# Kernel tuning notes

Hardware: AMD Instinct MI355X
Metric: run time of the kernel (lower is better)

Reference implementation:

```python
import jax, jax.numpy as jnp
import numpy as np

N = 100000      # nodes
E = 1600000     # edges
F_IN = 128
HID = 128
N_CLS = 40
KEEP = 0.5      # 1 - dropout p
NORM_BIAS = 0.0


def setup_inputs() -> dict:
    key = jax.random.key(0)
    ks = jax.random.split(key, 12)
    features = jax.random.normal(ks[0], (N, F_IN), jnp.float32)
    src = jax.random.randint(ks[1], (E,), 0, N, jnp.int32)
    dst = jax.random.randint(ks[2], (E,), 0, N, jnp.int32)
    mask1 = jax.random.randint(ks[3], (N, HID), 0, 2) == 1
    mask2 = jax.random.randint(ks[4], (N, HID), 0, 2) == 1
    # Glorot-ish weights, zero bias (as in DGL GraphConv defaults)
    w0 = jax.random.normal(ks[5], (F_IN, HID), jnp.float32) / np.sqrt(F_IN)
    b0 = jnp.zeros((HID,), jnp.float32)
    w1 = jax.random.normal(ks[6], (HID, HID), jnp.float32) / np.sqrt(HID)
    b1 = jnp.zeros((HID,), jnp.float32)
    w2 = jax.random.normal(ks[7], (HID, N_CLS), jnp.float32) / np.sqrt(HID)
    b2 = jnp.zeros((N_CLS,), jnp.float32)
    return {"features": features, "src": src, "dst": dst,
            "mask1": mask1, "mask2": mask2,
            "w0": w0, "b0": b0, "w1": w1, "b1": b1, "w2": w2, "b2": b2}


def _graph_conv(h, w, b, src, dst, norm, act):
    # GraphConv: linear -> SpMM (sum over in-edges) -> right norm -> bias -> act
    h = h @ w                                       # [N, d_out]
    agg = jax.ops.segment_sum(h[src], dst, num_segments=N)  # copy_u/sum SpMM
    h = agg * norm[:, None] + b
    return jax.nn.relu(h) if act else h


def reference(features, src, dst, mask1, mask2, w0, b0, w1, b1, w2, b2):
    # right normalization: 1 / (in_degree + norm_bias), degree clamped to >= 1
    deg = jax.ops.segment_sum(jnp.ones((E,), jnp.float32), dst, num_segments=N)
    norm = 1.0 / (jnp.maximum(deg, 1.0) + NORM_BIAS)

    h = _graph_conv(features, w0, b0, src, dst, norm, act=True)
    h = jnp.where(mask1, h / KEEP, 0.0)   # dropout (inverted, deterministic mask)
    h = _graph_conv(h, w1, b1, src, dst, norm, act=True)
    h = jnp.where(mask2, h / KEEP, 0.0)
    h = _graph_conv(h, w2, b2, src, dst, norm, act=False)
    return h
```

## Files before the change

### kernel.cpp

```cpp
#include <hip/hip_runtime.h>


#define PAD 64

__device__ __forceinline__ unsigned short f2bf(float f) {
    unsigned u = __float_as_uint(f);
    return (unsigned short)((u + 0x7fffu + ((u >> 16) & 1u)) >> 16);
}

__global__ __launch_bounds__(256) void k_init(int* __restrict__ cnt, int n,
                                              const unsigned* __restrict__ m,
                                              int* __restrict__ flag) {
    int base = blockIdx.x * 1024 + threadIdx.x * 4;
#pragma unroll
    for (int j = 0; j < 4; ++j) {
        int i = base + j;
        if (i < n) cnt[i] = 0;
    }
    if (blockIdx.x < 4) {
        unsigned v = m[blockIdx.x * 256 + threadIdx.x];
        if (v > 1u) atomicOr(flag, 1);
    }
}

__global__ __launch_bounds__(256) void k_g0scat(
        const float* __restrict__ X, const float* __restrict__ Wg,
        unsigned short* __restrict__ Y, int nrows, int gb,
        const int* __restrict__ src, const int* __restrict__ dst,
        int* __restrict__ cnt, int* __restrict__ slots, int E) {
    __shared__ float Xs[64][32];
    __shared__ float Ws[32][128];
    int bid = blockIdx.x;
    int t = threadIdx.x;

    bool isg = (bid < gb * 5) && ((bid % 5) == 4);
    if (!isg) {
        int sblk = (bid < gb * 5) ? (bid / 5) * 4 + (bid % 5)
                                  : gb * 4 + (bid - gb * 5);
        int e = sblk * 256 + t;
        if (e < E) {
            int d = dst[e];
            int p = atomicAdd(&cnt[d], 1);
            if (p < PAD) slots[(size_t)d * PAD + p] = src[e];
        }
        return;
    }

    int bm = (bid / 5) * 64;
    int tx = t & 15, ty = t >> 4;
    int sw = ((ty >> 1) & 3) << 2;
    float acc[4][8];
#pragma unroll
    for (int i = 0; i < 4; ++i)
#pragma unroll
        for (int j = 0; j < 8; ++j) acc[i][j] = 0.0f;

    for (int kc = 0; kc < 128; kc += 32) {
        for (int idx = t; idx < 64 * 8; idx += 256) {
            int row = idx >> 3, k4 = idx & 7;
            int grow = bm + row;
            if (grow >= nrows) grow = nrows - 1;
            float4 v = *(const float4*)(X + (size_t)grow * 128 + kc + k4 * 4);
            int kk2 = (k4 * 4) ^ (((row >> 3) & 3) << 2);
            *(float4*)&Xs[row][kk2] = v;
        }
        for (int idx = t; idx < 32 * 32; idx += 256) {
            int k = idx >> 5, c4 = idx & 31;
            *(float4*)&Ws[k][c4 * 4] =
                *(const float4*)(Wg + (size_t)(kc + k) * 128 + c4 * 4);
        }
        __syncthreads();

        for (int k = 0; k < 32; k += 4) {
            float4 a4[4];
#pragma unroll
            for (int i = 0; i < 4; ++i)
                a4[i] = *(const float4*)&Xs[ty * 4 + i][k ^ sw];
#pragma unroll
            for (int kk = 0; kk < 4; ++kk) {
                float b[8];
                *(float4*)&b[0] = *(const float4*)&Ws[k + kk][tx * 4];
                *(float4*)&b[4] = *(const float4*)&Ws[k + kk][64 + tx * 4];
#pragma unroll
                for (int i = 0; i < 4; ++i) {
                    float a = ((const float*)&a4[i])[kk];
#pragma unroll
                    for (int j = 0; j < 8; ++j) acc[i][j] += a * b[j];
                }
            }
        }
        __syncthreads();
    }

#pragma unroll
    for (int i = 0; i < 4; ++i) {
        int r = bm + ty * 4 + i;
        if (r < nrows) {
            ushort4 u0, u1;
            u0.x = f2bf(acc[i][0]); u0.y = f2bf(acc[i][1]);
            u0.z = f2bf(acc[i][2]); u0.w = f2bf(acc[i][3]);
            u1.x = f2bf(acc[i][4]); u1.y = f2bf(acc[i][5]);
            u1.z = f2bf(acc[i][6]); u1.w = f2bf(acc[i][7]);
            *(ushort4*)(Y + (size_t)r * 128 + tx * 4) = u0;
            *(ushort4*)(Y + (size_t)r * 128 + 64 + tx * 4) = u1;
        }
    }
}

template<int BN, bool PACK>
__global__ __launch_bounds__(256, 3) void k_gemm(const float* __restrict__ X,
                                                 const float* __restrict__ Wg,
                                                 unsigned short* __restrict__ Y,
                                                 int nrows, int wcols) {
    constexpr int TN = BN / 16;
    __shared__ float Xs[128][32];
    __shared__ float Ws[32][BN];
    int t = threadIdx.x;
    int bm = blockIdx.x * 128;
    int tx = t & 15, ty = t >> 4;
    int sw = (ty & 3) << 2;

    float acc[8][TN];
#pragma unroll
    for (int i = 0; i < 8; ++i)
#pragma unroll
        for (int j = 0; j < TN; ++j) acc[i][j] = 0.0f;

    for (int kc = 0; kc < 128; kc += 32) {
        for (int idx = t; idx < 128 * 8; idx += 256) {
            int row = idx >> 3, k4 = idx & 7;
            int grow = bm + row;
            if (grow >= nrows) grow = nrows - 1;
            float4 v = *(const float4*)(X + (size_t)grow * 128 + kc + k4 * 4);
            int kk2 = (k4 * 4) ^ (((row >> 3) & 3) << 2);
            *(float4*)&Xs[row][kk2] = v;
        }
        if (BN == 128) {
            for (int idx = t; idx < 32 * 32; idx += 256) {
                int k = idx >> 5, c4 = idx & 31;
                *(float4*)&Ws[k][c4 * 4] =
                    *(const float4*)(Wg + (size_t)(kc + k) * 128 + c4 * 4);
            }
        } else {
            for (int idx = t; idx < 32 * BN; idx += 256) {
                int k = idx / BN, c = idx % BN;
                Ws[k][c] = (c < wcols) ? Wg[(size_t)(kc + k) * wcols + c] : 0.0f;
            }
        }
        __syncthreads();

        for (int k = 0; k < 32; k += 4) {
            float4 a4[8];
#pragma unroll
            for (int i = 0; i < 8; ++i)
                a4[i] = *(const float4*)&Xs[ty * 8 + i][k ^ sw];
#pragma unroll
            for (int kk = 0; kk < 4; ++kk) {
                float b[TN];
                *(float4*)&b[0] = *(const float4*)&Ws[k + kk][tx * 4];
                if (BN == 128)
                    *(float4*)&b[4] = *(const float4*)&Ws[k + kk][64 + tx * 4];
#pragma unroll
                for (int i = 0; i < 8; ++i) {
                    float a = ((const float*)&a4[i])[kk];
#pragma unroll
                    for (int j = 0; j < TN; ++j) acc[i][j] += a * b[j];
                }
            }
        }
        __syncthreads();
    }

    int ld = PACK ? wcols : BN;
#pragma unroll
    for (int i = 0; i < 8; ++i) {
        int r = bm + ty * 8 + i;
        if (r < nrows) {
            if (!PACK || tx * 4 < 40) {
                ushort4 u;
                u.x = f2bf(acc[i][0]); u.y = f2bf(acc[i][1]);
                u.z = f2bf(acc[i][2]); u.w = f2bf(acc[i][3]);
                *(ushort4*)(Y + (size_t)r * ld + tx * 4) = u;
            }
            if (BN == 128) {
                ushort4 u;
                u.x = f2bf(acc[i][4]); u.y = f2bf(acc[i][5]);
                u.z = f2bf(acc[i][6]); u.w = f2bf(acc[i][7]);
                *(ushort4*)(Y + (size_t)r * ld + 64 + tx * 4) = u;
            }
        }
    }
}

template<bool ACT>
__global__ __launch_bounds__(256) void k_spmmw(const unsigned* __restrict__ Y,
                       const int* __restrict__ cnt, const int* __restrict__ slots,
                       const float* __restrict__ bias,
                       const void* __restrict__ mask, const int* __restrict__ mflag,
                       float* __restrict__ H, int N) {
    int wid = threadIdx.x >> 6;
    int lane = threadIdx.x & 63;
    int i = blockIdx.x * 4 + wid;
    if (i >= N) return;
    int c = lane * 2;
    int d0 = cnt[i];
    int d = d0 > PAD ? PAD : d0;
    const int* row = slots + (size_t)i * PAD;
    float2 acc = {0.0f, 0.0f};
    int e = 0;
    for (; e + 3 < d; e += 4) {
        unsigned u0 = Y[(size_t)row[e] * 64 + lane];
        unsigned u1 = Y[(size_t)row[e + 1] * 64 + lane];
        unsigned u2 = Y[(size_t)row[e + 2] * 64 + lane];
        unsigned u3 = Y[(size_t)row[e + 3] * 64 + lane];
        acc.x += __uint_as_float(u0 << 16) + __uint_as_float(u1 << 16)
               + __uint_as_float(u2 << 16) + __uint_as_float(u3 << 16);
        acc.y += __uint_as_float(u0 & 0xffff0000u) + __uint_as_float(u1 & 0xffff0000u)
               + __uint_as_float(u2 & 0xffff0000u) + __uint_as_float(u3 & 0xffff0000u);
    }
    for (; e < d; ++e) {
        unsigned u = Y[(size_t)row[e] * 64 + lane];
        acc.x += __uint_as_float(u << 16);
        acc.y += __uint_as_float(u & 0xffff0000u);
    }
    float nrm = 1.0f / fmaxf((float)d0, 1.0f);
    float2 b = *(const float2*)&bias[c];
    float vx = acc.x * nrm + b.x;
    float vy = acc.y * nrm + b.y;
    if (ACT) {
        vx = fmaxf(vx, 0.0f);
        vy = fmaxf(vy, 0.0f);
        size_t j = (size_t)i * 128 + c;
        bool k0, k1;
        if (*mflag != 0) {
            const unsigned char* m = (const unsigned char*)mask;
            k0 = m[j] != 0; k1 = m[j + 1] != 0;
        } else {
            const int* m = (const int*)mask;
            k0 = m[j] != 0; k1 = m[j + 1] != 0;
        }
        vx = k0 ? vx * 2.0f : 0.0f;
        vy = k1 ? vy * 2.0f : 0.0f;
    }
    *(float2*)(H + (size_t)i * 128 + c) = make_float2(vx, vy);
}

__global__ __launch_bounds__(256) void k_spmm40w(const unsigned* __restrict__ Y,
                        const int* __restrict__ cnt, const int* __restrict__ slots,
                        const float* __restrict__ bias,
                        float* __restrict__ H, int N, int width) {
    int wid = threadIdx.x >> 6;
    int lane = threadIdx.x & 63;
    int i = blockIdx.x * 4 + wid;
    if (i >= N) return;
    int c = lane * 2;
    if (c >= width) return;
    int d0 = cnt[i];
    int d = d0 > PAD ? PAD : d0;
    const int* row = slots + (size_t)i * PAD;
    float2 acc = {0.0f, 0.0f};
    int e = 0;
    for (; e + 3 < d; e += 4) {
        unsigned u0 = Y[(size_t)row[e] * 20 + lane];
        unsigned u1 = Y[(size_t)row[e + 1] * 20 + lane];
        unsigned u2 = Y[(size_t)row[e + 2] * 20 + lane];
        unsigned u3 = Y[(size_t)row[e + 3] * 20 + lane];
        acc.x += __uint_as_float(u0 << 16) + __uint_as_float(u1 << 16)
               + __uint_as_float(u2 << 16) + __uint_as_float(u3 << 16);
        acc.y += __uint_as_float(u0 & 0xffff0000u) + __uint_as_float(u1 & 0xffff0000u)
               + __uint_as_float(u2 & 0xffff0000u) + __uint_as_float(u3 & 0xffff0000u);
    }
    for (; e < d; ++e) {
        unsigned u = Y[(size_t)row[e] * 20 + lane];
        acc.x += __uint_as_float(u << 16);
        acc.y += __uint_as_float(u & 0xffff0000u);
    }
    float nrm = 1.0f / fmaxf((float)d0, 1.0f);
    float vx = acc.x * nrm + bias[c];
    float vy = acc.y * nrm + bias[c + 1];
    *(float2*)(H + (size_t)i * width + c) = make_float2(vx, vy);
}

extern "C" void kernel_launch(void* const* d_in, const int* in_sizes, int n_in,
                              void* d_out, int out_size, void* d_ws, size_t ws_size,
                              hipStream_t stream) {
    const float* feat = (const float*)d_in[0];
    const int* src = (const int*)d_in[1];
    const int* dst = (const int*)d_in[2];
    const void* mask1 = d_in[3];
    const void* mask2 = d_in[4];
    const float* w0 = (const float*)d_in[5];
    const float* b0 = (const float*)d_in[6];
    const float* w1 = (const float*)d_in[7];
    const float* b1 = (const float*)d_in[8];
    const float* w2 = (const float*)d_in[9];
    const float* b2 = (const float*)d_in[10];
    int N = in_sizes[0] / 128;
    int E = in_sizes[1];
    int ncls = in_sizes[10];

    float* out = (float*)d_out;
    unsigned short* Y = (unsigned short*)d_ws;
    float* H = (float*)(Y + (size_t)N * 128);
    int* slots = (int*)(H + (size_t)N * 128);
    int* cnt = slots + (size_t)N * PAD;
    int* mflag = cnt + N;

    int nb = (N + 1023) / 1024;

    hipMemsetAsync(mflag, 0, 4, stream);
    k_init<<<nb, 256, 0, stream>>>(cnt, N, (const unsigned*)mask1, mflag);

    int eb = (E + 255) / 256;
    int gb64 = (N + 63) / 64;
    int scap = gb64 * 4;
    int extra = (eb > scap) ? (eb - scap) : 0;
    k_g0scat<<<gb64 * 5 + extra, 256, 0, stream>>>(feat, w0, Y, N, gb64,
                                                   src, dst, cnt, slots, E);

    int gb = (N + 127) / 128;
    int sb = (N + 3) / 4;
    k_spmmw<true><<<sb, 256, 0, stream>>>((const unsigned*)Y, cnt, slots, b0, mask1, mflag, H, N);
    k_gemm<128, false><<<gb, 256, 0, stream>>>(H, w1, Y, N, 128);
    k_spmmw<true><<<sb, 256, 0, stream>>>((const unsigned*)Y, cnt, slots, b1, mask2, mflag, H, N);
    k_gemm<64, true><<<gb, 256, 0, stream>>>(H, w2, Y, N, ncls);
    k_spmm40w<<<sb, 256, 0, stream>>>((const unsigned*)Y, cnt, slots, b2, out, N, ncls);
}
```

Measured before the change: 440.3 us.

## Shard edge scatter by destination range aligned to XCDs for L2 locality

Edge bucketing is restructured so each scatter block handles a 2048-edge window but only inserts edges whose destination lies in one of 8 node shards. The shard is picked as bid%8, which appears to line up with round-robin block placement across the 8 XCDs, so each XCD's atomics and slot writes stay within its own L2 slice. The cost is that every edge's dst is read 8 times, once per shard, and the block-to-window mapping becomes more complex. The hardcoded shard size of 12500 ties correctness to N=100000; for any larger N, nodes beyond the last shard would never be inserted.

```diff
diff --git a/kernel.cpp b/kernel.cpp
--- a/kernel.cpp
+++ b/kernel.cpp
@@ -2,6 +2,9 @@
 
 
 #define PAD 64
+#define NSHARD 8
+#define SHARD_DIV 12500
+#define WIN 2048
 
 __device__ __forceinline__ unsigned short f2bf(float f) {
     unsigned u = __float_as_uint(f);
@@ -25,7 +28,7 @@
 
 __global__ __launch_bounds__(256) void k_g0scat(
         const float* __restrict__ X, const float* __restrict__ Wg,
-        unsigned short* __restrict__ Y, int nrows, int gb,
+        unsigned short* __restrict__ Y, int nrows, int nwin,
         const int* __restrict__ src, const int* __restrict__ dst,
         int* __restrict__ cnt, int* __restrict__ slots, int E) {
     __shared__ float Xs[64][32];
@@ -33,20 +36,32 @@
     int bid = blockIdx.x;
     int t = threadIdx.x;
 
-    bool isg = (bid < gb * 5) && ((bid % 5) == 4);
-    if (!isg) {
-        int sblk = (bid < gb * 5) ? (bid / 5) * 4 + (bid % 5)
-                                  : gb * 4 + (bid - gb * 5);
-        int e = sblk * 256 + t;
-        if (e < E) {
-            int d = dst[e];
-            int p = atomicAdd(&cnt[d], 1);
-            if (p < PAD) slots[(size_t)d * PAD + p] = src[e];
+    if ((bid % 5) != 4) {
+        int q = bid % 40;
+        int rank = 0;
+        for (int j = bid % 8; j < q; j += 8)
+            if ((j % 5) != 4) ++rank;
+        int w = (bid / 40) * 4 + rank;
+        if (w >= nwin) return;
+        int shard = bid % 8;
+        int lo = shard * SHARD_DIV, hi = lo + SHARD_DIV;
+        int base = w * WIN + t;
+#pragma unroll
+        for (int k = 0; k < 8; ++k) {
+            int e = base + k * 256;
+            if (e < E) {
+                int d = dst[e];
+                if (d >= lo && d < hi) {
+                    int p = atomicAdd(&cnt[d], 1);
+                    if (p < PAD) slots[(size_t)d * PAD + p] = src[e];
+                }
+            }
         }
         return;
     }
 
     int bm = (bid / 5) * 64;
+    if (bm >= nrows) return;
     int tx = t & 15, ty = t >> 4;
     int sw = ((ty >> 1) & 3) << 2;
     float acc[4][8];
@@ -311,12 +326,13 @@
     hipMemsetAsync(mflag, 0, 4, stream);
     k_init<<<nb, 256, 0, stream>>>(cnt, N, (const unsigned*)mask1, mflag);
 
-    int eb = (E + 255) / 256;
+    int nwin = (E + WIN - 1) / WIN;
     int gb64 = (N + 63) / 64;
-    int scap = gb64 * 4;
-    int extra = (eb > scap) ? (eb - scap) : 0;
-    k_g0scat<<<gb64 * 5 + extra, 256, 0, stream>>>(feat, w0, Y, N, gb64,
-                                                   src, dst, cnt, slots, E);
+    int sp1 = (nwin * 8 + 31) / 32;
+    int sp2 = (gb64 + 7) / 8;
+    int sp = sp1 > sp2 ? sp1 : sp2;
+    k_g0scat<<<sp * 40, 256, 0, stream>>>(feat, w0, Y, N, nwin,
+                                          src, dst, cnt, slots, E);
 
     int gb = (N + 127) / 128;
     int sb = (N + 3) / 4;
```

Measured after the change: 436.1 us. About the same (-1.0%).

## Fuse SpMM aggregation with following dense GEMM via shared-memory tile

Applied to the files above, without the earlier changes.

Replaces the separate SpMM kernel (which wrote an fp32 H matrix) and the following GEMM kernel with a single kernel. Each block aggregates 64 destination rows, applies norm, bias, ReLU and the dropout mask, and stores the result in a swizzled 64x128 shared tile. It then multiplies that tile by the weight matrix and writes bf16 output. This removes the global write and re-read of the N x 128 fp32 intermediate and two launches. The cost is larger shared memory per block (32KB+), which lowers occupancy for the latency-bound gather phase, and smaller GEMM tiles.

```diff
diff --git a/kernel.cpp b/kernel.cpp
--- a/kernel.cpp
+++ b/kernel.cpp
@@ -107,34 +107,76 @@
     }
 }
 
-template<int BN, bool PACK>
-__global__ __launch_bounds__(256, 3) void k_gemm(const float* __restrict__ X,
-                                                 const float* __restrict__ Wg,
-                                                 unsigned short* __restrict__ Y,
-                                                 int nrows, int wcols) {
+template<int BN>
+__global__ __launch_bounds__(256) void k_spgemm(
+        const unsigned* __restrict__ Yin,
+        const int* __restrict__ cnt, const int* __restrict__ slots,
+        const float* __restrict__ bias,
+        const void* __restrict__ mask, const int* __restrict__ mflag,
+        const float* __restrict__ Wg,
+        unsigned short* __restrict__ Yout, int N, int wcols) {
     constexpr int TN = BN / 16;
-    __shared__ float Xs[128][32];
+    __shared__ float Xs[64][128];
     __shared__ float Ws[32][BN];
     int t = threadIdx.x;
-    int bm = blockIdx.x * 128;
+    int bm = blockIdx.x * 64;
+    int wid = t >> 6, lane = t & 63;
+    int c = lane * 2;
+    bool bytemask = (*mflag != 0);
+
+    for (int n = 0; n < 16; ++n) {
+        int row = wid * 16 + n;
+        int i = bm + row;
+        if (i >= N) break;
+        int d0 = cnt[i];
+        int d = d0 > PAD ? PAD : d0;
+        const int* rw = slots + (size_t)i * PAD;
+        float2 acc = {0.0f, 0.0f};
+        int e = 0;
+        for (; e + 3 < d; e += 4) {
+            unsigned u0 = Yin[(size_t)rw[e] * 64 + lane];
+            unsigned u1 = Yin[(size_t)rw[e + 1] * 64 + lane];
+            unsigned u2 = Yin[(size_t)rw[e + 2] * 64 + lane];
+            unsigned u3 = Yin[(size_t)rw[e + 3] * 64 + lane];
+            acc.x += __uint_as_float(u0 << 16) + __uint_as_float(u1 << 16)
+                   + __uint_as_float(u2 << 16) + __uint_as_float(u3 << 16);
+            acc.y += __uint_as_float(u0 & 0xffff0000u) + __uint_as_float(u1 & 0xffff0000u)
+                   + __uint_as_float(u2 & 0xffff0000u) + __uint_as_float(u3 & 0xffff0000u);
+        }
+        for (; e < d; ++e) {
+            unsigned u = Yin[(size_t)rw[e] * 64 + lane];
+            acc.x += __uint_as_float(u << 16);
+            acc.y += __uint_as_float(u & 0xffff0000u);
+        }
+        float nrm = 1.0f / fmaxf((float)d0, 1.0f);
+        float2 b = *(const float2*)&bias[c];
+        float vx = fmaxf(acc.x * nrm + b.x, 0.0f);
+        float vy = fmaxf(acc.y * nrm + b.y, 0.0f);
+        size_t j = (size_t)i * 128 + c;
+        bool k0, k1;
+        if (bytemask) {
+            const unsigned char* m = (const unsigned char*)mask;
+            k0 = m[j] != 0; k1 = m[j + 1] != 0;
+        } else {
+            const int* m = (const int*)mask;
+            k0 = m[j] != 0; k1 = m[j + 1] != 0;
+        }
+        vx = k0 ? vx * 2.0f : 0.0f;
+        vy = k1 ? vy * 2.0f : 0.0f;
+        int swr = ((row >> 2) & 3) << 2;
+        *(float2*)&Xs[row][c ^ swr] = make_float2(vx, vy);
+    }
+    __syncthreads();
+
     int tx = t & 15, ty = t >> 4;
     int sw = (ty & 3) << 2;
-
-    float acc[8][TN];
-#pragma unroll
-    for (int i = 0; i < 8; ++i)
+    float acc[4][TN];
+#pragma unroll
+    for (int i = 0; i < 4; ++i)
 #pragma unroll
         for (int j = 0; j < TN; ++j) acc[i][j] = 0.0f;
 
     for (int kc = 0; kc < 128; kc += 32) {
-        for (int idx = t; idx < 128 * 8; idx += 256) {
-            int row = idx >> 3, k4 = idx & 7;
-            int grow = bm + row;
-            if (grow >= nrows) grow = nrows - 1;
-            float4 v = *(const float4*)(X + (size_t)grow * 128 + kc + k4 * 4);
-            int kk2 = (k4 * 4) ^ (((row >> 3) & 3) << 2);
-            *(float4*)&Xs[row][kk2] = v;
-        }
         if (BN == 128) {
             for (int idx = t; idx < 32 * 32; idx += 256) {
                 int k = idx >> 5, c4 = idx & 31;
@@ -143,17 +185,17 @@
             }
         } else {
             for (int idx = t; idx < 32 * BN; idx += 256) {
-                int k = idx / BN, c = idx % BN;
-                Ws[k][c] = (c < wcols) ? Wg[(size_t)(kc + k) * wcols + c] : 0.0f;
+                int k = idx / BN, cc = idx % BN;
+                Ws[k][cc] = (cc < wcols) ? Wg[(size_t)(kc + k) * wcols + cc] : 0.0f;
             }
         }
         __syncthreads();
 
         for (int k = 0; k < 32; k += 4) {
-            float4 a4[8];
-#pragma unroll
-            for (int i = 0; i < 8; ++i)
-                a4[i] = *(const float4*)&Xs[ty * 8 + i][k ^ sw];
+            float4 a4[4];
+#pragma unroll
+            for (int i = 0; i < 4; ++i)
+                a4[i] = *(const float4*)&Xs[ty * 4 + i][(kc + k) ^ sw];
 #pragma unroll
             for (int kk = 0; kk < 4; ++kk) {
                 float b[TN];
@@ -161,7 +203,7 @@
                 if (BN == 128)
                     *(float4*)&b[4] = *(const float4*)&Ws[k + kk][64 + tx * 4];
 #pragma unroll
-                for (int i = 0; i < 8; ++i) {
+                for (int i = 0; i < 4; ++i) {
                     float a = ((const float*)&a4[i])[kk];
 #pragma unroll
                     for (int j = 0; j < TN; ++j) acc[i][j] += a * b[j];
@@ -171,78 +213,25 @@
         __syncthreads();
     }
 
-    int ld = PACK ? wcols : BN;
-#pragma unroll
-    for (int i = 0; i < 8; ++i) {
-        int r = bm + ty * 8 + i;
-        if (r < nrows) {
-            if (!PACK || tx * 4 < 40) {
+    int ld = (BN == 128) ? 128 : wcols;
+#pragma unroll
+    for (int i = 0; i < 4; ++i) {
+        int r = bm + ty * 4 + i;
+        if (r < N) {
+            if (BN == 128 || tx * 4 < 40) {
                 ushort4 u;
                 u.x = f2bf(acc[i][0]); u.y = f2bf(acc[i][1]);
                 u.z = f2bf(acc[i][2]); u.w = f2bf(acc[i][3]);
-                *(ushort4*)(Y + (size_t)r * ld + tx * 4) = u;
+                *(ushort4*)(Yout + (size_t)r * ld + tx * 4) = u;
             }
             if (BN == 128) {
                 ushort4 u;
                 u.x = f2bf(acc[i][4]); u.y = f2bf(acc[i][5]);
                 u.z = f2bf(acc[i][6]); u.w = f2bf(acc[i][7]);
-                *(ushort4*)(Y + (size_t)r * ld + 64 + tx * 4) = u;
-            }
-        }
-    }
-}
-
-template<bool ACT>
-__global__ __launch_bounds__(256) void k_spmmw(const unsigned* __restrict__ Y,
-                       const int* __restrict__ cnt, const int* __restrict__ slots,
-                       const float* __restrict__ bias,
-                       const void* __restrict__ mask, const int* __restrict__ mflag,
-                       float* __restrict__ H, int N) {
-    int wid = threadIdx.x >> 6;
-    int lane = threadIdx.x & 63;
-    int i = blockIdx.x * 4 + wid;
-    if (i >= N) return;
-    int c = lane * 2;
-    int d0 = cnt[i];
-    int d = d0 > PAD ? PAD : d0;
-    const int* row = slots + (size_t)i * PAD;
-    float2 acc = {0.0f, 0.0f};
-    int e = 0;
-    for (; e + 3 < d; e += 4) {
-        unsigned u0 = Y[(size_t)row[e] * 64 + lane];
-        unsigned u1 = Y[(size_t)row[e + 1] * 64 + lane];
-        unsigned u2 = Y[(size_t)row[e + 2] * 64 + lane];
-        unsigned u3 = Y[(size_t)row[e + 3] * 64 + lane];
-        acc.x += __uint_as_float(u0 << 16) + __uint_as_float(u1 << 16)
-               + __uint_as_float(u2 << 16) + __uint_as_float(u3 << 16);
-        acc.y += __uint_as_float(u0 & 0xffff0000u) + __uint_as_float(u1 & 0xffff0000u)
-               + __uint_as_float(u2 & 0xffff0000u) + __uint_as_float(u3 & 0xffff0000u);
-    }
-    for (; e < d; ++e) {
-        unsigned u = Y[(size_t)row[e] * 64 + lane];
-        acc.x += __uint_as_float(u << 16);
-        acc.y += __uint_as_float(u & 0xffff0000u);
-    }
-    float nrm = 1.0f / fmaxf((float)d0, 1.0f);
-    float2 b = *(const float2*)&bias[c];
-    float vx = acc.x * nrm + b.x;
-    float vy = acc.y * nrm + b.y;
-    if (ACT) {
-        vx = fmaxf(vx, 0.0f);
-        vy = fmaxf(vy, 0.0f);
-        size_t j = (size_t)i * 128 + c;
-        bool k0, k1;
-        if (*mflag != 0) {
-            const unsigned char* m = (const unsigned char*)mask;
-            k0 = m[j] != 0; k1 = m[j + 1] != 0;
-        } else {
-            const int* m = (const int*)mask;
-            k0 = m[j] != 0; k1 = m[j + 1] != 0;
-        }
-        vx = k0 ? vx * 2.0f : 0.0f;
-        vy = k1 ? vy * 2.0f : 0.0f;
-    }
-    *(float2*)(H + (size_t)i * 128 + c) = make_float2(vx, vy);
+                *(ushort4*)(Yout + (size_t)r * ld + 64 + tx * 4) = u;
+            }
+        }
+    }
 }
 
 __global__ __launch_bounds__(256) void k_spmm40w(const unsigned* __restrict__ Y,
@@ -300,9 +289,10 @@
     int ncls = in_sizes[10];
 
     float* out = (float*)d_out;
-    unsigned short* Y = (unsigned short*)d_ws;
-    float* H = (float*)(Y + (size_t)N * 128);
-    int* slots = (int*)(H + (size_t)N * 128);
+    unsigned short* Y0 = (unsigned short*)d_ws;
+    unsigned short* Y1 = Y0 + (size_t)N * 128;
+    unsigned short* Y40 = Y0;
+    int* slots = (int*)(Y1 + (size_t)N * 128);
     int* cnt = slots + (size_t)N * PAD;
     int* mflag = cnt + N;
 
@@ -315,14 +305,15 @@
     int gb64 = (N + 63) / 64;
     int scap = gb64 * 4;
     int extra = (eb > scap) ? (eb - scap) : 0;
-    k_g0scat<<<gb64 * 5 + extra, 256, 0, stream>>>(feat, w0, Y, N, gb64,
+    k_g0scat<<<gb64 * 5 + extra, 256, 0, stream>>>(feat, w0, Y0, N, gb64,
                                                    src, dst, cnt, slots, E);
 
-    int gb = (N + 127) / 128;
+    k_spgemm<128><<<gb64, 256, 0, stream>>>((const unsigned*)Y0, cnt, slots,
+                                            b0, mask1, mflag, w1, Y1, N, 128);
+    k_spgemm<64><<<gb64, 256, 0, stream>>>((const unsigned*)Y1, cnt, slots,
+                                           b1, mask2, mflag, w2, Y40, N, ncls);
+
     int sb = (N + 3) / 4;
-    k_spmmw<true><<<sb, 256, 0, stream>>>((const unsigned*)Y, cnt, slots, b0, mask1, mflag, H, N);
-    k_gemm<128, false><<<gb, 256, 0, stream>>>(H, w1, Y, N, 128);
-    k_spmmw<true><<<sb, 256, 0, stream>>>((const unsigned*)Y, cnt, slots, b1, mask2, mflag, H, N);
-    k_gemm<64, true><<<gb, 256, 0, stream>>>(H, w2, Y, N, ncls);
-    k_spmm40w<<<sb, 256, 0, stream>>>((const unsigned*)Y, cnt, slots, b2, out, N, ncls);
-}
+    k_spmm40w<<<sb, 256, 0, stream>>>((const unsigned*)Y40, cnt, slots, b2,
+                                      out, N, ncls);
+}
```

After: 609.1 us. +38.3%, slower.

## Use bf16 MFMA for hidden GEMMs and store SpMM activations as bf16

Applied to the files above, without the earlier changes.

Replaces the fp32 FMA tiled GEMMs for layers 1 and 2 with a bf16 MFMA kernel (16x16x32) that loads swizzled bf16 tiles into shared memory. The weights are pre-transposed and converted to bf16 inside the init kernel. The SpMM now writes packed bf16 activations instead of fp32, which halves the intermediate write and GEMM read traffic. This adds a second rounding of the activations to bf16 before the GEMM, a small precision risk.

```diff
diff --git a/kernel.cpp b/kernel.cpp
--- a/kernel.cpp
+++ b/kernel.cpp
@@ -2,6 +2,9 @@
 
 
 #define PAD 64
+
+typedef short short8 __attribute__((ext_vector_type(8)));
+typedef float f32x4 __attribute__((ext_vector_type(4)));
 
 __device__ __forceinline__ unsigned short f2bf(float f) {
     unsigned u = __float_as_uint(f);
@@ -10,7 +13,11 @@
 
 __global__ __launch_bounds__(256) void k_init(int* __restrict__ cnt, int n,
                                               const unsigned* __restrict__ m,
-                                              int* __restrict__ flag) {
+                                              int* __restrict__ flag,
+                                              const float* __restrict__ W1,
+                                              const float* __restrict__ W2,
+                                              unsigned short* __restrict__ W1T,
+                                              unsigned short* __restrict__ W2T) {
     int base = blockIdx.x * 1024 + threadIdx.x * 4;
 #pragma unroll
     for (int j = 0; j < 4; ++j) {
@@ -20,6 +27,15 @@
     if (blockIdx.x < 4) {
         unsigned v = m[blockIdx.x * 256 + threadIdx.x];
         if (v > 1u) atomicOr(flag, 1);
+    }
+    int g = blockIdx.x * 256 + threadIdx.x;
+    if (g < 128 * 128) {
+        int k = g >> 7, c = g & 127;
+        W1T[c * 128 + k] = f2bf(W1[g]);
+    }
+    if (g < 48 * 128) {
+        int c = g >> 7, k = g & 127;
+        W2T[g] = (c < 40) ? f2bf(W2[k * 40 + c]) : (unsigned short)0;
     }
 }
 
@@ -107,97 +123,70 @@
     }
 }
 
-template<int BN, bool PACK>
-__global__ __launch_bounds__(256, 3) void k_gemm(const float* __restrict__ X,
-                                                 const float* __restrict__ Wg,
-                                                 unsigned short* __restrict__ Y,
-                                                 int nrows, int wcols) {
-    constexpr int TN = BN / 16;
-    __shared__ float Xs[128][32];
-    __shared__ float Ws[32][BN];
+template<int BN>
+__global__ __launch_bounds__(256) void k_mfma(
+        const unsigned short* __restrict__ Xg,
+        const unsigned short* __restrict__ WT,
+        unsigned short* __restrict__ Yout, int N, int ldo) {
+    constexpr int CT = BN / 16;
+    __shared__ unsigned short Xs[128][128];
+    __shared__ unsigned short Ws[BN][128];
     int t = threadIdx.x;
     int bm = blockIdx.x * 128;
-    int tx = t & 15, ty = t >> 4;
-    int sw = (ty & 3) << 2;
-
-    float acc[8][TN];
-#pragma unroll
-    for (int i = 0; i < 8; ++i)
-#pragma unroll
-        for (int j = 0; j < TN; ++j) acc[i][j] = 0.0f;
-
-    for (int kc = 0; kc < 128; kc += 32) {
-        for (int idx = t; idx < 128 * 8; idx += 256) {
-            int row = idx >> 3, k4 = idx & 7;
-            int grow = bm + row;
-            if (grow >= nrows) grow = nrows - 1;
-            float4 v = *(const float4*)(X + (size_t)grow * 128 + kc + k4 * 4);
-            int kk2 = (k4 * 4) ^ (((row >> 3) & 3) << 2);
-            *(float4*)&Xs[row][kk2] = v;
-        }
-        if (BN == 128) {
-            for (int idx = t; idx < 32 * 32; idx += 256) {
-                int k = idx >> 5, c4 = idx & 31;
-                *(float4*)&Ws[k][c4 * 4] =
-                    *(const float4*)(Wg + (size_t)(kc + k) * 128 + c4 * 4);
+
+    for (int idx = t; idx < 128 * 16; idx += 256) {
+        int row = idx >> 4, c = idx & 15;
+        int grow = bm + row;
+        if (grow >= N) grow = N - 1;
+        uint4 v = *(const uint4*)(Xg + (size_t)grow * 128 + c * 8);
+        *(uint4*)&Xs[row][(c ^ (row & 15)) * 8] = v;
+    }
+    for (int idx = t; idx < BN * 16; idx += 256) {
+        int row = idx >> 4, c = idx & 15;
+        uint4 v = *(const uint4*)(WT + (size_t)row * 128 + c * 8);
+        *(uint4*)&Ws[row][(c ^ (row & 15)) * 8] = v;
+    }
+    __syncthreads();
+
+    int l = t & 63, w = t >> 6;
+    int lr = l & 15, lg = l >> 4;
+    f32x4 acc[2][CT];
+#pragma unroll
+    for (int rt = 0; rt < 2; ++rt)
+#pragma unroll
+        for (int ct = 0; ct < CT; ++ct) acc[rt][ct] = (f32x4)0.0f;
+
+#pragma unroll
+    for (int ks = 0; ks < 4; ++ks) {
+        int cc = (ks * 4 + lg) ^ lr;
+        short8 a0 = *(const short8*)&Xs[w * 32 + lr][cc * 8];
+        short8 a1 = *(const short8*)&Xs[w * 32 + 16 + lr][cc * 8];
+#pragma unroll
+        for (int ct = 0; ct < CT; ++ct) {
+            short8 b = *(const short8*)&Ws[ct * 16 + lr][cc * 8];
+            acc[0][ct] = __builtin_amdgcn_mfma_f32_16x16x32_bf16(a0, b, acc[0][ct], 0, 0, 0);
+            acc[1][ct] = __builtin_amdgcn_mfma_f32_16x16x32_bf16(a1, b, acc[1][ct], 0, 0, 0);
+        }
+    }
+
+#pragma unroll
+    for (int rt = 0; rt < 2; ++rt)
+#pragma unroll
+        for (int ct = 0; ct < CT; ++ct)
+#pragma unroll
+            for (int i = 0; i < 4; ++i) {
+                int r = bm + w * 32 + rt * 16 + lg * 4 + i;
+                int col = ct * 16 + lr;
+                if (r < N && (BN == 128 || col < 40))
+                    Yout[(size_t)r * ldo + col] = f2bf(acc[rt][ct][i]);
             }
-        } else {
-            for (int idx = t; idx < 32 * BN; idx += 256) {
-                int k = idx / BN, c = idx % BN;
-                Ws[k][c] = (c < wcols) ? Wg[(size_t)(kc + k) * wcols + c] : 0.0f;
-            }
-        }
-        __syncthreads();
-
-        for (int k = 0; k < 32; k += 4) {
-            float4 a4[8];
-#pragma unroll
-            for (int i = 0; i < 8; ++i)
-                a4[i] = *(const float4*)&Xs[ty * 8 + i][k ^ sw];
-#pragma unroll
-            for (int kk = 0; kk < 4; ++kk) {
-                float b[TN];
-                *(float4*)&b[0] = *(const float4*)&Ws[k + kk][tx * 4];
-                if (BN == 128)
-                    *(float4*)&b[4] = *(const float4*)&Ws[k + kk][64 + tx * 4];
-#pragma unroll
-                for (int i = 0; i < 8; ++i) {
-                    float a = ((const float*)&a4[i])[kk];
-#pragma unroll
-                    for (int j = 0; j < TN; ++j) acc[i][j] += a * b[j];
-                }
-            }
-        }
-        __syncthreads();
-    }
-
-    int ld = PACK ? wcols : BN;
-#pragma unroll
-    for (int i = 0; i < 8; ++i) {
-        int r = bm + ty * 8 + i;
-        if (r < nrows) {
-            if (!PACK || tx * 4 < 40) {
-                ushort4 u;
-                u.x = f2bf(acc[i][0]); u.y = f2bf(acc[i][1]);
-                u.z = f2bf(acc[i][2]); u.w = f2bf(acc[i][3]);
-                *(ushort4*)(Y + (size_t)r * ld + tx * 4) = u;
-            }
-            if (BN == 128) {
-                ushort4 u;
-                u.x = f2bf(acc[i][4]); u.y = f2bf(acc[i][5]);
-                u.z = f2bf(acc[i][6]); u.w = f2bf(acc[i][7]);
-                *(ushort4*)(Y + (size_t)r * ld + 64 + tx * 4) = u;
-            }
-        }
-    }
-}
-
-template<bool ACT>
+}
+
 __global__ __launch_bounds__(256) void k_spmmw(const unsigned* __restrict__ Y,
                        const int* __restrict__ cnt, const int* __restrict__ slots,
                        const float* __restrict__ bias,
                        const void* __restrict__ mask, const int* __restrict__ mflag,
-                       float* __restrict__ H, int N) {
+                       unsigned* __restrict__ H, int N) {
     int wid = threadIdx.x >> 6;
     int lane = threadIdx.x & 63;
     int i = blockIdx.x * 4 + wid;
@@ -225,24 +214,21 @@
     }
     float nrm = 1.0f / fmaxf((float)d0, 1.0f);
     float2 b = *(const float2*)&bias[c];
-    float vx = acc.x * nrm + b.x;
-    float vy = acc.y * nrm + b.y;
-    if (ACT) {
-        vx = fmaxf(vx, 0.0f);
-        vy = fmaxf(vy, 0.0f);
-        size_t j = (size_t)i * 128 + c;
-        bool k0, k1;
-        if (*mflag != 0) {
-            const unsigned char* m = (const unsigned char*)mask;
-            k0 = m[j] != 0; k1 = m[j + 1] != 0;
-        } else {
-            const int* m = (const int*)mask;
-            k0 = m[j] != 0; k1 = m[j + 1] != 0;
-        }
-        vx = k0 ? vx * 2.0f : 0.0f;
-        vy = k1 ? vy * 2.0f : 0.0f;
-    }
-    *(float2*)(H + (size_t)i * 128 + c) = make_float2(vx, vy);
+    float vx = fmaxf(acc.x * nrm + b.x, 0.0f);
+    float vy = fmaxf(acc.y * nrm + b.y, 0.0f);
+    size_t j = (size_t)i * 128 + c;
+    bool k0, k1;
+    if (*mflag != 0) {
+        const unsigned char* m = (const unsigned char*)mask;
+        k0 = m[j] != 0; k1 = m[j + 1] != 0;
+    } else {
+        const int* m = (const int*)mask;
+        k0 = m[j] != 0; k1 = m[j + 1] != 0;
+    }
+    vx = k0 ? vx * 2.0f : 0.0f;
+    vy = k1 ? vy * 2.0f : 0.0f;
+    H[(size_t)i * 64 + lane] =
+        (unsigned)f2bf(vx) | ((unsigned)f2bf(vy) << 16);
 }
 
 __global__ __launch_bounds__(256) void k_spmm40w(const unsigned* __restrict__ Y,
@@ -300,29 +286,35 @@
     int ncls = in_sizes[10];
 
     float* out = (float*)d_out;
-    unsigned short* Y = (unsigned short*)d_ws;
-    float* H = (float*)(Y + (size_t)N * 128);
-    int* slots = (int*)(H + (size_t)N * 128);
+    unsigned short* A = (unsigned short*)d_ws;
+    unsigned short* B = A + (size_t)N * 128;
+    int* slots = (int*)(B + (size_t)N * 128);
     int* cnt = slots + (size_t)N * PAD;
     int* mflag = cnt + N;
+    unsigned short* W1T = (unsigned short*)(cnt + N + 4);
+    unsigned short* W2T = W1T + 128 * 128;
 
     int nb = (N + 1023) / 1024;
 
     hipMemsetAsync(mflag, 0, 4, stream);
-    k_init<<<nb, 256, 0, stream>>>(cnt, N, (const unsigned*)mask1, mflag);
+    k_init<<<nb, 256, 0, stream>>>(cnt, N, (const unsigned*)mask1, mflag,
+                                   w1, w2, W1T, W2T);
 
     int eb = (E + 255) / 256;
     int gb64 = (N + 63) / 64;
     int scap = gb64 * 4;
     int extra = (eb > scap) ? (eb - scap) : 0;
-    k_g0scat<<<gb64 * 5 + extra, 256, 0, stream>>>(feat, w0, Y, N, gb64,
+    k_g0scat<<<gb64 * 5 + extra, 256, 0, stream>>>(feat, w0, A, N, gb64,
                                                    src, dst, cnt, slots, E);
 
-    int gb = (N + 127) / 128;
+    int gb128 = (N + 127) / 128;
     int sb = (N + 3) / 4;
-    k_spmmw<true><<<sb, 256, 0, stream>>>((const unsigned*)Y, cnt, slots, b0, mask1, mflag, H, N);
-    k_gemm<128, false><<<gb, 256, 0, stream>>>(H, w1, Y, N, 128);
-    k_spmmw<true><<<sb, 256, 0, stream>>>((const unsigned*)Y, cnt, slots, b1, mask2, mflag, H, N);
-    k_gemm<64, true><<<gb, 256, 0, stream>>>(H, w2, Y, N, ncls);
-    k_spmm40w<<<sb, 256, 0, stream>>>((const unsigned*)Y, cnt, slots, b2, out, N, ncls);
-}
+    k_spmmw<<<sb, 256, 0, stream>>>((const unsigned*)A, cnt, slots, b0,
+                                    mask1, mflag, (unsigned*)B, N);
+    k_mfma<128><<<gb128, 256, 0, stream>>>(B, W1T, A, N, 128);
+    k_spmmw<<<sb, 256, 0, stream>>>((const unsigned*)A, cnt, slots, b1,
+                                    mask2, mflag, (unsigned*)B, N);
+    k_mfma<48><<<gb128, 256, 0, stream>>>(B, W2T, A, N, ncls);
+    k_spmm40w<<<sb, 256, 0, stream>>>((const unsigned*)A, cnt, slots, b2,
+                                      out, N, ncls);
+}
```

New measurement: 357.1 us. 1.23x faster.
